# Performance work log

Measured on AMD Instinct MI355X. Metric: run time of the kernel, lower is better.

The kernel has to match this reference:

```python
import jax, jax.numpy as jnp
import numpy as np

N_SIN = 3  # fcn_n_sin

def _feats(x):
    # x: [B, Din] -> features [B, Din, 1 + 2*N_SIN]
    omega = (2.0 ** jnp.arange(N_SIN, dtype=x.dtype))  # [n_sin]
    ox = x[..., None] * omega  # [B, Din, n_sin]
    return jnp.concatenate([x[..., None], jnp.sin(ox), jnp.cos(ox)], axis=-1)

def setup_inputs() -> dict:
    key = jax.random.key(0)
    k1, k2, k3 = jax.random.split(key, 3)
    B, Din, Dout, H, F = 2048, 64, 64, 32, 1 + 2 * N_SIN
    x = jax.random.normal(k1, (B, Din), dtype=jnp.float32)
    # xavier-normal-ish init for W1/W2, zeros for biases (matches init_parameters)
    W1 = jax.random.normal(k2, (Din, Dout, H, F), dtype=jnp.float32) * np.sqrt(2.0 / (H + F))
    W2 = jax.random.normal(k3, (Din, Dout, 1, H), dtype=jnp.float32) * np.sqrt(2.0 / (1 + H))
    B1 = jnp.zeros((Din, Dout, H), dtype=jnp.float32)
    B2 = jnp.zeros((Din, Dout, 1), dtype=jnp.float32)
    return {"x": x, "W1": W1, "W2": W2, "B1": B1, "B2": B2}

def reference(x, W1, W2, B1, B2):
    f = _feats(x)  # [B, Din, F]
    # per-edge first layer: [B, Din, Dout, H]
    h = jnp.einsum('bif,iohf->bioh', f, W1) + B1[None]
    h = jax.nn.silu(h)
    # per-edge second layer -> scalar: [B, Din, Dout]
    phis = jnp.einsum('bioh,ioh->bio', h, W2[:, :, 0, :]) + B2[:, :, 0][None]
    return phis.sum(axis=1)  # [B, Dout]
```

## Files before the change

### kernel.cpp

```cpp
#include <hip/hip_runtime.h>
#include <math.h>

typedef _Float16 f16;
typedef f16   f16x8    __attribute__((ext_vector_type(8)));
typedef float floatx4  __attribute__((ext_vector_type(4)));
typedef float floatx16 __attribute__((ext_vector_type(16)));

#define LOG2E 1.44269504088896340736f

#define B_SZ  2048
#define DIN   64
#define DOUT  64
#define NH    32

#define NIG   4
#define IGW   (DIN / NIG)

#define W1IMG_ELEMS ((size_t)DIN * DOUT * 64 * 8)
#define FIMG_ELEMS  ((size_t)DIN * 64 * 64 * 8)
#define W2Q_ELEMS   ((size_t)DIN * DOUT * NH)

__global__ __launch_bounds__(256) void prep_kernel(
        const float* __restrict__ W1, const float* __restrict__ B1,
        const float* __restrict__ W2, const float* __restrict__ B2,
        const float* __restrict__ x,
        f16* __restrict__ w1img, f16* __restrict__ fimg,
        float* __restrict__ w2q, float* __restrict__ b2sum) {
    const int bid = blockIdx.x, tid = threadIdx.x;
    if (bid < 1024) {
        int e = bid * 256 + tid;
        int lane = e & 63, o = (e >> 6) & 63, i = e >> 12;
        f16x8 v = {};
        if (lane < 32) {
            const float* w = W1 + (size_t)((i * 64 + o) * 32 + lane) * 7;
#pragma unroll
            for (int j = 0; j < 7; ++j) v[j] = (f16)(w[j] * (-LOG2E));
            v[7] = (f16)(B1[(i * 64 + o) * 32 + lane] * (-LOG2E));
        }
        *(f16x8*)(w1img + (size_t)e * 8) = v;
    } else if (bid < 2048) {
        int e = (bid - 1024) * 256 + tid;
        int lane = e & 63, btp = (e >> 6) & 63, i = e >> 12;
        f16x8 v = {};
        if (lane < 32) {
            int b = btp * 32 + lane;
            float xv = x[b * 64 + i];
            float s1, c1;
            __sincosf(xv, &s1, &c1);
            float s2 = 2.0f * s1 * c1, c2 = 1.0f - 2.0f * s1 * s1;
            float s4 = 2.0f * s2 * c2, c4 = 1.0f - 2.0f * s2 * s2;
            v[0] = (f16)xv; v[1] = (f16)s1; v[2] = (f16)s2; v[3] = (f16)s4;
            v[4] = (f16)c1; v[5] = (f16)c2; v[6] = (f16)c4; v[7] = (f16)1.0f;
        }
        *(f16x8*)(fimg + (size_t)e * 8) = v;
    } else if (bid < 2560) {
        int e = (bid - 2048) * 256 + tid;
        int r = e & 3, p = (e >> 2) & 1, q = (e >> 3) & 3;
        int o = (e >> 5) & 63, i = e >> 11;
        int h = q * 8 + p * 4 + r;
        w2q[e] = W2[(size_t)(i * 64 + o) * 32 + h] * (-1.0f / LOG2E);
    } else if (tid < 64) {
        float s = 0.0f;
        for (int i = 0; i < 64; ++i) s += B2[i * 64 + tid];
        b2sum[tid] = s;
    }
}

__global__ __launch_bounds__(128, 4) void main_kernel(
        const f16* __restrict__ w1img, const f16* __restrict__ fimg,
        const float* __restrict__ w2q, float* __restrict__ partials) {
    const int tid  = threadIdx.x;
    const int lane = tid & 63;
    const int wv   = tid >> 6;
    const int btp  = blockIdx.x & 63;
    const int og   = (blockIdx.x >> 6) & 31;
    const int ig   = blockIdx.x >> 11;
    const int o    = __builtin_amdgcn_readfirstlane(og * 2 + wv);
    const int p    = lane >> 5;

    const size_t ibase = (size_t)ig * IGW;
    const f16*   ap = w1img + ibase * 32768 + ((size_t)o * 64 + lane) * 8;
    const f16*   bp = fimg  + ibase * 32768 + ((size_t)btp * 64 + lane) * 8;
    const float* wp = w2q   + ibase * 2048  + (size_t)o * 32 + p * 4;

    f16x8 a = *(const f16x8*)ap;
    f16x8 b = *(const f16x8*)bp;
    floatx4 w0 = *(const floatx4*)(wp);
    floatx4 w1 = *(const floatx4*)(wp + 8);
    floatx4 w2 = *(const floatx4*)(wp + 16);
    floatx4 w3 = *(const floatx4*)(wp + 24);

    float phi = 0.0f;
    const floatx16 zeroC = {};

#pragma unroll 1
    for (int ii = 0; ii < IGW; ++ii) {
        const f16x8 ca = a, cb = b;
        const floatx4 cw0 = w0, cw1 = w1, cw2 = w2, cw3 = w3;

        const size_t i1 = (size_t)(ii + 1);
        a  = *(const f16x8*)(ap + i1 * 32768);
        b  = *(const f16x8*)(bp + i1 * 32768);
        w0 = *(const floatx4*)(wp + i1 * 2048);
        w1 = *(const floatx4*)(wp + i1 * 2048 + 8);
        w2 = *(const floatx4*)(wp + i1 * 2048 + 16);
        w3 = *(const floatx4*)(wp + i1 * 2048 + 24);

        floatx16 C = __builtin_amdgcn_mfma_f32_32x32x16_f16(ca, cb, zeroC, 0, 0, 0);

#pragma unroll
        for (int r = 0; r < 4; ++r) {
            float av, e2, sg;
            av = C[0 + r];  e2 = __builtin_amdgcn_exp2f(av);
            sg = __builtin_amdgcn_rcpf(1.0f + e2);
            phi = __builtin_fmaf(av * cw0[r], sg, phi);
            av = C[4 + r];  e2 = __builtin_amdgcn_exp2f(av);
            sg = __builtin_amdgcn_rcpf(1.0f + e2);
            phi = __builtin_fmaf(av * cw1[r], sg, phi);
            av = C[8 + r];  e2 = __builtin_amdgcn_exp2f(av);
            sg = __builtin_amdgcn_rcpf(1.0f + e2);
            phi = __builtin_fmaf(av * cw2[r], sg, phi);
            av = C[12 + r]; e2 = __builtin_amdgcn_exp2f(av);
            sg = __builtin_amdgcn_rcpf(1.0f + e2);
            phi = __builtin_fmaf(av * cw3[r], sg, phi);
        }
    }

    phi += __shfl_xor(phi, 32, 64);

    if (lane < 32) {
        partials[((size_t)ig * B_SZ + btp * 32 + lane) * 64 + o] = phi;
    }
}

__global__ __launch_bounds__(256) void reduce_kernel(
        const float* __restrict__ partials, const float* __restrict__ b2sum,
        float* __restrict__ out) {
    int t = blockIdx.x * 256 + threadIdx.x;
    floatx4 s = *(const floatx4*)(b2sum + ((t * 4) & 63));
#pragma unroll
    for (int gg = 0; gg < NIG; ++gg) {
        floatx4 v = *(const floatx4*)(partials + (size_t)gg * (B_SZ * DOUT) + t * 4);
        s += v;
    }
    *(floatx4*)(out + (size_t)t * 4) = s;
}

extern "C" void kernel_launch(void* const* d_in, const int* in_sizes, int n_in,
                              void* d_out, int out_size, void* d_ws, size_t ws_size,
                              hipStream_t stream) {
    const float* x  = (const float*)d_in[0];
    const float* W1 = (const float*)d_in[1];
    const float* W2 = (const float*)d_in[2];
    const float* B1 = (const float*)d_in[3];
    const float* B2 = (const float*)d_in[4];
    float* out = (float*)d_out;

    f16*   w1img    = (f16*)d_ws;
    f16*   fimg     = w1img + W1IMG_ELEMS;
    float* w2q      = (float*)(fimg + FIMG_ELEMS);
    float* b2sum    = w2q + W2Q_ELEMS;
    float* partials = b2sum + 64;

    prep_kernel<<<2561, 256, 0, stream>>>(W1, B1, W2, B2, x, w1img, fimg, w2q, b2sum);
    main_kernel<<<NIG * 32 * 64, 128, 0, stream>>>(w1img, fimg, w2q, partials);
    reduce_kernel<<<(B_SZ * DOUT) / 1024, 256, 0, stream>>>(partials, b2sum, out);
}
```

Before: 129.1 us.

## Use 32x32x8 MFMA with half-size images, LDS W2 staging, atomic output reduction

Switches from the K=16 MFMA with zero-padded f16x8 operands to the K=8 variant with packed f16x4 operands, halving the size of the W1 and feature images and the global traffic in the main loop. W2 coefficients for the block are staged once into shared memory instead of being prefetched from global each iteration. The reduce kernel and partials buffer are replaced by atomic adds into an output that prep zeroes, with the bias split across the four input groups. Four independent accumulators shorten the FMA dependency chain. The atomics add contention and make the summation order nondeterministic.

```diff
diff --git a/kernel.cpp b/kernel.cpp
--- a/kernel.cpp
+++ b/kernel.cpp
@@ -2,6 +2,7 @@
 #include <math.h>
 
 typedef _Float16 f16;
+typedef f16   f16x4    __attribute__((ext_vector_type(4)));
 typedef f16   f16x8    __attribute__((ext_vector_type(8)));
 typedef float floatx4  __attribute__((ext_vector_type(4)));
 typedef float floatx16 __attribute__((ext_vector_type(16)));
@@ -16,8 +17,8 @@
 #define NIG   4
 #define IGW   (DIN / NIG)
 
-#define W1IMG_ELEMS ((size_t)DIN * DOUT * 64 * 8)
-#define FIMG_ELEMS  ((size_t)DIN * 64 * 64 * 8)
+#define W1IMG_ELEMS ((size_t)DIN * DOUT * 64 * 4)
+#define FIMG_ELEMS  ((size_t)DIN * 64 * 64 * 4)
 #define W2Q_ELEMS   ((size_t)DIN * DOUT * NH)
 
 __global__ __launch_bounds__(256) void prep_kernel(
@@ -25,40 +26,61 @@
         const float* __restrict__ W2, const float* __restrict__ B2,
         const float* __restrict__ x,
         f16* __restrict__ w1img, f16* __restrict__ fimg,
-        float* __restrict__ w2q, float* __restrict__ b2sum) {
+        float* __restrict__ w2q, float* __restrict__ b2sum,
+        float* __restrict__ out) {
     const int bid = blockIdx.x, tid = threadIdx.x;
-    if (bid < 1024) {
-        int e = bid * 256 + tid;
-        int lane = e & 63, o = (e >> 6) & 63, i = e >> 12;
-        f16x8 v = {};
-        if (lane < 32) {
-            const float* w = W1 + (size_t)((i * 64 + o) * 32 + lane) * 7;
+    if (bid < 512) {
+        int u = bid * 256 + tid;
+        int lane2 = u & 31, o = (u >> 5) & 63, i = u >> 11;
+        int l0 = lane2 * 2;
+        f16x8 v;
+        if (lane2 < 16) {
 #pragma unroll
-            for (int j = 0; j < 7; ++j) v[j] = (f16)(w[j] * (-LOG2E));
-            v[7] = (f16)(B1[(i * 64 + o) * 32 + lane] * (-LOG2E));
+            for (int t = 0; t < 2; ++t) {
+                const float* w = W1 + (size_t)((i * 64 + o) * 32 + l0 + t) * 7;
+#pragma unroll
+                for (int j = 0; j < 4; ++j) v[t * 4 + j] = (f16)(w[j] * (-LOG2E));
+            }
+        } else {
+#pragma unroll
+            for (int t = 0; t < 2; ++t) {
+                int m = l0 - 32 + t;
+                const float* w = W1 + (size_t)((i * 64 + o) * 32 + m) * 7;
+                v[t * 4 + 0] = (f16)(w[4] * (-LOG2E));
+                v[t * 4 + 1] = (f16)(w[5] * (-LOG2E));
+                v[t * 4 + 2] = (f16)(w[6] * (-LOG2E));
+                v[t * 4 + 3] = (f16)(B1[(i * 64 + o) * 32 + m] * (-LOG2E));
+            }
         }
-        *(f16x8*)(w1img + (size_t)e * 8) = v;
-    } else if (bid < 2048) {
-        int e = (bid - 1024) * 256 + tid;
-        int lane = e & 63, btp = (e >> 6) & 63, i = e >> 12;
-        f16x8 v = {};
-        if (lane < 32) {
-            int b = btp * 32 + lane;
+        *(f16x8*)(w1img + (size_t)u * 8) = v;
+    } else if (bid < 1024) {
+        int u = (bid - 512) * 256 + tid;
+        int lane2 = u & 31, btp = (u >> 5) & 63, i = u >> 11;
+        int l0 = lane2 * 2;
+        f16x8 v;
+#pragma unroll
+        for (int t = 0; t < 2; ++t) {
+            int b = btp * 32 + ((l0 + t) & 31);
             float xv = x[b * 64 + i];
             float s1, c1;
             __sincosf(xv, &s1, &c1);
             float s2 = 2.0f * s1 * c1, c2 = 1.0f - 2.0f * s1 * s1;
             float s4 = 2.0f * s2 * c2, c4 = 1.0f - 2.0f * s2 * s2;
-            v[0] = (f16)xv; v[1] = (f16)s1; v[2] = (f16)s2; v[3] = (f16)s4;
-            v[4] = (f16)c1; v[5] = (f16)c2; v[6] = (f16)c4; v[7] = (f16)1.0f;
+            if (lane2 < 16) { v[t*4+0] = (f16)xv; v[t*4+1] = (f16)s1;
+                              v[t*4+2] = (f16)s2; v[t*4+3] = (f16)s4; }
+            else            { v[t*4+0] = (f16)c1; v[t*4+1] = (f16)c2;
+                              v[t*4+2] = (f16)c4; v[t*4+3] = (f16)1.0f; }
         }
-        *(f16x8*)(fimg + (size_t)e * 8) = v;
-    } else if (bid < 2560) {
-        int e = (bid - 2048) * 256 + tid;
-        int r = e & 3, p = (e >> 2) & 1, q = (e >> 3) & 3;
-        int o = (e >> 5) & 63, i = e >> 11;
-        int h = q * 8 + p * 4 + r;
-        w2q[e] = W2[(size_t)(i * 64 + o) * 32 + h] * (-1.0f / LOG2E);
+        *(f16x8*)(fimg + (size_t)u * 8) = v;
+    } else if (bid < 1152) {
+        int t = (bid - 1024) * 256 + tid;
+        floatx4 v = *(const floatx4*)(W2 + (size_t)t * 4);
+        v *= (-1.0f / LOG2E);
+        *(floatx4*)(w2q + (size_t)t * 4) = v;
+    } else if (bid < 1280) {
+        int t = (bid - 1152) * 256 + tid;
+        floatx4 z = {};
+        *(floatx4*)(out + (size_t)t * 4) = z;
     } else if (tid < 64) {
         float s = 0.0f;
         for (int i = 0; i < 64; ++i) s += B2[i * 64 + tid];
@@ -68,7 +90,8 @@
 
 __global__ __launch_bounds__(128, 4) void main_kernel(
         const f16* __restrict__ w1img, const f16* __restrict__ fimg,
-        const float* __restrict__ w2q, float* __restrict__ partials) {
+        const float* __restrict__ w2q, const float* __restrict__ b2sum,
+        float* __restrict__ out) {
     const int tid  = threadIdx.x;
     const int lane = tid & 63;
     const int wv   = tid >> 6;
@@ -77,73 +100,69 @@
     const int ig   = blockIdx.x >> 11;
     const int o    = __builtin_amdgcn_readfirstlane(og * 2 + wv);
     const int p    = lane >> 5;
+    const size_t ibase = (size_t)ig * IGW;
 
-    const size_t ibase = (size_t)ig * IGW;
-    const f16*   ap = w1img + ibase * 32768 + ((size_t)o * 64 + lane) * 8;
-    const f16*   bp = fimg  + ibase * 32768 + ((size_t)btp * 64 + lane) * 8;
-    const float* wp = w2q   + ibase * 2048  + (size_t)o * 32 + p * 4;
+    __shared__ float ws2[2][IGW][32];
+    {
+        int idx = tid * 8;
+        int wv_ = idx >> 9, ii_ = (idx >> 5) & 15, h_ = idx & 31;
+        const float* src = w2q + (ibase + ii_) * 2048
+                         + (size_t)(og * 2 + wv_) * 32 + h_;
+        *(floatx4*)&ws2[wv_][ii_][h_]     = *(const floatx4*)src;
+        *(floatx4*)&ws2[wv_][ii_][h_ + 4] = *(const floatx4*)(src + 4);
+    }
+    __syncthreads();
 
-    f16x8 a = *(const f16x8*)ap;
-    f16x8 b = *(const f16x8*)bp;
-    floatx4 w0 = *(const floatx4*)(wp);
-    floatx4 w1 = *(const floatx4*)(wp + 8);
-    floatx4 w2 = *(const floatx4*)(wp + 16);
-    floatx4 w3 = *(const floatx4*)(wp + 24);
+    const f16* ap = w1img + ibase * 16384 + ((size_t)o   * 64 + lane) * 4;
+    const f16* bp = fimg  + ibase * 16384 + ((size_t)btp * 64 + lane) * 4;
 
-    float phi = 0.0f;
+    f16x4 a = *(const f16x4*)ap;
+    f16x4 b = *(const f16x4*)bp;
+
+    float phi0 = 0.0f, phi1 = 0.0f, phi2 = 0.0f, phi3 = 0.0f;
     const floatx16 zeroC = {};
 
 #pragma unroll 1
     for (int ii = 0; ii < IGW; ++ii) {
-        const f16x8 ca = a, cb = b;
-        const floatx4 cw0 = w0, cw1 = w1, cw2 = w2, cw3 = w3;
+        const f16x4 ca = a, cb = b;
 
         const size_t i1 = (size_t)(ii + 1);
-        a  = *(const f16x8*)(ap + i1 * 32768);
-        b  = *(const f16x8*)(bp + i1 * 32768);
-        w0 = *(const floatx4*)(wp + i1 * 2048);
-        w1 = *(const floatx4*)(wp + i1 * 2048 + 8);
-        w2 = *(const floatx4*)(wp + i1 * 2048 + 16);
-        w3 = *(const floatx4*)(wp + i1 * 2048 + 24);
+        a = *(const f16x4*)(ap + i1 * 16384);
+        b = *(const f16x4*)(bp + i1 * 16384);
 
-        floatx16 C = __builtin_amdgcn_mfma_f32_32x32x16_f16(ca, cb, zeroC, 0, 0, 0);
+        const float* wrow = &ws2[wv][ii][p * 4];
+        const floatx4 cw0 = *(const floatx4*)(wrow);
+        const floatx4 cw1 = *(const floatx4*)(wrow + 8);
+        const floatx4 cw2 = *(const floatx4*)(wrow + 16);
+        const floatx4 cw3 = *(const floatx4*)(wrow + 24);
+
+        floatx16 C = __builtin_amdgcn_mfma_f32_32x32x8f16(ca, cb, zeroC, 0, 0, 0);
 
 #pragma unroll
         for (int r = 0; r < 4; ++r) {
             float av, e2, sg;
             av = C[0 + r];  e2 = __builtin_amdgcn_exp2f(av);
             sg = __builtin_amdgcn_rcpf(1.0f + e2);
-            phi = __builtin_fmaf(av * cw0[r], sg, phi);
+            phi0 = __builtin_fmaf(av * cw0[r], sg, phi0);
             av = C[4 + r];  e2 = __builtin_amdgcn_exp2f(av);
             sg = __builtin_amdgcn_rcpf(1.0f + e2);
-            phi = __builtin_fmaf(av * cw1[r], sg, phi);
+            phi1 = __builtin_fmaf(av * cw1[r], sg, phi1);
             av = C[8 + r];  e2 = __builtin_amdgcn_exp2f(av);
             sg = __builtin_amdgcn_rcpf(1.0f + e2);
-            phi = __builtin_fmaf(av * cw2[r], sg, phi);
+            phi2 = __builtin_fmaf(av * cw2[r], sg, phi2);
             av = C[12 + r]; e2 = __builtin_amdgcn_exp2f(av);
             sg = __builtin_amdgcn_rcpf(1.0f + e2);
-            phi = __builtin_fmaf(av * cw3[r], sg, phi);
+            phi3 = __builtin_fmaf(av * cw3[r], sg, phi3);
         }
     }
 
+    float phi = (phi0 + phi1) + (phi2 + phi3);
     phi += __shfl_xor(phi, 32, 64);
 
     if (lane < 32) {
-        partials[((size_t)ig * B_SZ + btp * 32 + lane) * 64 + o] = phi;
+        float v = phi + 0.25f * b2sum[o];
+        unsafeAtomicAdd(out + (size_t)(btp * 32 + lane) * 64 + o, v);
     }
-}
-
-__global__ __launch_bounds__(256) void reduce_kernel(
-        const float* __restrict__ partials, const float* __restrict__ b2sum,
-        float* __restrict__ out) {
-    int t = blockIdx.x * 256 + threadIdx.x;
-    floatx4 s = *(const floatx4*)(b2sum + ((t * 4) & 63));
-#pragma unroll
-    for (int gg = 0; gg < NIG; ++gg) {
-        floatx4 v = *(const floatx4*)(partials + (size_t)gg * (B_SZ * DOUT) + t * 4);
-        s += v;
-    }
-    *(floatx4*)(out + (size_t)t * 4) = s;
 }
 
 extern "C" void kernel_launch(void* const* d_in, const int* in_sizes, int n_in,
@@ -156,13 +175,11 @@
     const float* B2 = (const float*)d_in[4];
     float* out = (float*)d_out;
 
-    f16*   w1img    = (f16*)d_ws;
-    f16*   fimg     = w1img + W1IMG_ELEMS;
-    float* w2q      = (float*)(fimg + FIMG_ELEMS);
-    float* b2sum    = w2q + W2Q_ELEMS;
-    float* partials = b2sum + 64;
+    f16*   w1img = (f16*)d_ws;
+    f16*   fimg  = w1img + W1IMG_ELEMS;
+    float* w2q   = (float*)(fimg + FIMG_ELEMS);
+    float* b2sum = w2q + W2Q_ELEMS;
 
-    prep_kernel<<<2561, 256, 0, stream>>>(W1, B1, W2, B2, x, w1img, fimg, w2q, b2sum);
-    main_kernel<<<NIG * 32 * 64, 128, 0, stream>>>(w1img, fimg, w2q, partials);
-    reduce_kernel<<<(B_SZ * DOUT) / 1024, 256, 0, stream>>>(partials, b2sum, out);
+    prep_kernel<<<1281, 256, 0, stream>>>(W1, B1, W2, B2, x, w1img, fimg, w2q, b2sum, out);
+    main_kernel<<<NIG * 32 * 64, 128, 0, stream>>>(w1img, fimg, w2q, b2sum, out);
 }
```

Result: no change. 128.6 us (-0.4%).
